# Kernel tuning notes

Measured on AMD Instinct MI355X. Metric: run time of the kernel, lower is better.

Reference implementation:

```python
import jax, jax.numpy as jnp
import numpy as np

N, DEG, FIN, FOUT, K = 50000, 16, 32, 64, 3
E = N * DEG


def setup_inputs() -> dict:
    key = jax.random.key(0)
    ks = jax.random.split(key, 10)
    rng = np.random.default_rng(0)
    # unique edges sorted row-major (src*N+dst), ring guarantees deg_in/out>0
    ring = np.arange(N, dtype=np.int64) * N + (np.arange(N, dtype=np.int64) + 1) % N
    cand = np.unique(rng.integers(0, N * N, size=3 * E, dtype=np.int64))
    cand = np.setdiff1d(cand, ring, assume_unique=True)[: E - N]
    codes = np.sort(np.concatenate([cand, ring]))
    assert codes.shape[0] == E
    edge_index = jnp.asarray(np.stack([codes // N, codes % N]).astype(np.int32))
    X = jax.random.normal(ks[0], (N, FIN), jnp.float32)
    edge_weight = jax.random.uniform(ks[1], (E,), jnp.float32, 0.5, 1.5)
    cin = FIN + FOUT
    xav = float(np.sqrt(6.0 / (cin + FOUT)))
    def w(k):
        return jax.random.uniform(k, (2, K, cin, FOUT), jnp.float32, -xav, xav)
    return {
        'X': X, 'edge_index': edge_index, 'edge_weight': edge_weight,
        'Wz': w(ks[2]), 'bz': jnp.zeros((FOUT,), jnp.float32),
        'Wr': w(ks[3]), 'br': jnp.zeros((FOUT,), jnp.float32),
        'Wh': w(ks[4]), 'bh': jnp.zeros((FOUT,), jnp.float32),
    }


def _dconv(X, src, dst, rev_src, rev_dst, norm_out, norm_in, W, b):
    n = X.shape[0]
    def prop(x, s, d, nrm):  # out[d] += nrm * x[s]
        return jax.ops.segment_sum(nrm[:, None] * x[s], d, num_segments=n)
    H = X @ W[0, 0] + X @ W[1, 0]
    if W.shape[1] > 1:
        Tx1o = prop(X, src, dst, norm_out)
        Tx1i = prop(X, rev_src, rev_dst, norm_in)
        H = H + Tx1o @ W[0, 1] + Tx1i @ W[1, 1]
        for k in range(2, W.shape[1]):
            Tx1o = 2.0 * prop(Tx1o, src, dst, norm_out) - X
            Tx1i = 2.0 * prop(Tx1i, rev_src, rev_dst, norm_in) - X
            H = H + Tx1o @ W[0, k] + Tx1i @ W[1, k]
    return H + b


def reference(X, edge_index, edge_weight, Wz, bz, Wr, br, Wh, bh):
    n = X.shape[0]
    src, dst = edge_index[0], edge_index[1]
    deg_out = jax.ops.segment_sum(edge_weight, src, num_segments=n)
    deg_in = jax.ops.segment_sum(edge_weight, dst, num_segments=n)
    # faithful to original: both norms indexed by row (source)
    norm_out = 1.0 / deg_out[src]
    norm_in = 1.0 / deg_in[src]
    # reverse edges in dense_to_sparse(adj.T) order: sorted by (dst, src)
    order = jnp.argsort(dst.astype(jnp.int64) * n + src.astype(jnp.int64))
    rev_src, rev_dst = dst[order], src[order]
    H = jnp.zeros((n, Wz.shape[-1]), X.dtype)
    dc = lambda inp, W, b: _dconv(inp, src, dst, rev_src, rev_dst, norm_out, norm_in, W, b)
    Z = jax.nn.sigmoid(dc(jnp.concatenate([X, H], axis=1), Wz, bz))
    R = jax.nn.sigmoid(dc(jnp.concatenate([X, H], axis=1), Wr, br))
    H_tilde = jnp.tanh(dc(jnp.concatenate([X, H * R], axis=1), Wh, bh))
    return Z * H + (1.0 - Z) * H_tilde
```

## Files before the change

### kernel.cpp

```cpp
#include <hip/hip_runtime.h>
#include <hip/hip_fp16.h>
#include <cmath>

#define NN 50000
#define NE 800000
#define PADF 96
#define NBIN 196
#define NBLK 391
#define FCAP 6144
#define DST_HI 42949
#define SRC_CUT 33648

__device__ __forceinline__ unsigned short f2h(float f) {
  __half h = __float2half_rn(f);
  return *reinterpret_cast<unsigned short*>(&h);
}

typedef _Float16 half4 __attribute__((ext_vector_type(4)));
typedef float f32x4 __attribute__((ext_vector_type(4)));

__global__ __launch_bounds__(256) void k_aux(const float* __restrict__ X, const int* __restrict__ src,
                                             const int* __restrict__ dst, const float* __restrict__ ew,
                                             int* __restrict__ H,
                                             int* __restrict__ rptr, float* __restrict__ dout,
                                             const float* __restrict__ Wz, const float* __restrict__ Wh,
                                             unsigned short* __restrict__ WT, unsigned short* __restrict__ Xh,
                                             int* __restrict__ s0g) {
  __shared__ int hh[256];
  __shared__ int s0l;
  int bid = blockIdx.x;
  int t = threadIdx.x;
  if (bid >= 667) {
    int h = bid - 667;
    hh[t] = 0;
    if (t == 0) s0l = 0;
    __syncthreads();
    int my = 0;
#pragma unroll
    for (int r = 0; r < 8; ++r) {
      int e = h * 2048 + r * 256 + t;
      if (e < NE) {
        int d = dst[e];
        atomicAdd(&hh[d >> 8], 1);
        my += (d < DST_HI) ? 1 : 0;
        my += (d == DST_HI && src[e] < SRC_CUT) ? 1 : 0;
      }
    }
    atomicAdd(&s0l, my);
    __syncthreads();
    if (t < NBIN) H[t * NBLK + h] = hh[t];
    if (t == 0) atomicAdd(s0g, s0l);
  } else if (bid < 196) {
    int i = bid * 256 + t;
    if (i >= NN) return;
    int lo = 0, hi = NE;
    while (lo < hi) { int m = (lo + hi) >> 1; if (src[m] < i) lo = m + 1; else hi = m; }
    int lo2 = lo, hi2 = NE;
    while (lo2 < hi2) { int m = (lo2 + hi2) >> 1; if (src[m] < i + 1) lo2 = m + 1; else hi2 = m; }
    rptr[i] = lo;
    if (i == NN - 1) rptr[NN] = lo2;
    float a = 0.f;
    for (int p = lo; p < lo2; ++p) a += ew[p];
    dout[i] = a;
  } else if (bid < 276) {
    int idx = (bid - 196) * 256 + t;
    int kk = idx >> 7, f = idx & 127;
    int blk = kk >> 5, c = kk & 31;
    const float* W = (f < 64) ? Wz : Wh;
    int fl = f & 63;
    float v;
    if (blk == 0)      v = W[c * 64 + fl] + W[18432 + c * 64 + fl];
    else if (blk == 1) v = W[6144 + c * 64 + fl];
    else if (blk == 2) v = W[18432 + 6144 + c * 64 + fl];
    else if (blk == 3) v = W[2 * 6144 + c * 64 + fl];
    else               v = W[18432 + 2 * 6144 + c * 64 + fl];
    WT[f * 160 + kk] = f2h(v);
  } else {
    int tt = (bid - 276) * 256 + t;
    int base = tt * 16;
    if (base >= NN * 32) return;
#pragma unroll
    for (int q = 0; q < 2; ++q) {
      const float4 a = *(const float4*)&X[base + q * 8];
      const float4 b = *(const float4*)&X[base + q * 8 + 4];
      ushort4 o1 = make_ushort4(f2h(a.x), f2h(a.y), f2h(a.z), f2h(a.w));
      ushort4 o2 = make_ushort4(f2h(b.x), f2h(b.y), f2h(b.z), f2h(b.w));
      *(ushort4*)&Xh[base + q * 8] = o1;
      *(ushort4*)&Xh[base + q * 8 + 4] = o2;
    }
  }
}

__global__ __launch_bounds__(512) void k_scanrow(int* __restrict__ H, int* __restrict__ rowtot) {
  __shared__ int tmp[512];
  int row = blockIdx.x;
  int t = threadIdx.x;
  int v = (t < NBLK) ? H[row * NBLK + t] : 0;
  tmp[t] = v;
  __syncthreads();
  for (int off = 1; off < 512; off <<= 1) {
    int u = (t >= (unsigned)off) ? tmp[t - off] : 0;
    __syncthreads();
    tmp[t] += u;
    __syncthreads();
  }
  if (t < NBLK) H[row * NBLK + t] = tmp[t] - v;
  if (t == 511) rowtot[row] = tmp[511];
}

__global__ __launch_bounds__(256) void k_part(const int* __restrict__ src, const int* __restrict__ dst,
                                              const int* __restrict__ P, const int* __restrict__ rowtot,
                                              unsigned long long* __restrict__ cmp64) {
  __shared__ int loc[NBIN];
  __shared__ int rs[256];
  __shared__ int rbase[NBIN];
  int h = blockIdx.x;
  int t = threadIdx.x;
  int v = (t < NBIN) ? rowtot[t] : 0;
  rs[t] = v;
  if (t < NBIN) loc[t] = 0;
  __syncthreads();
  for (int off = 1; off < 256; off <<= 1) {
    int u = (t >= (unsigned)off) ? rs[t - off] : 0;
    __syncthreads();
    rs[t] += u;
    __syncthreads();
  }
  if (t < NBIN) rbase[t] = rs[t] - v;
  __syncthreads();
#pragma unroll
  for (int r = 0; r < 8; ++r) {
    int e = h * 2048 + r * 256 + t;
    if (e < NE) {
      int d = dst[e];
      int bin = d >> 8;
      int rk = atomicAdd(&loc[bin], 1);
      int pos = rbase[bin] + P[bin * NBLK + h] + rk;
      cmp64[pos] = ((unsigned long long)(d & 255) << 48) |
                   ((unsigned long long)src[e] << 24) | (unsigned long long)e;
    }
  }
}

__global__ __launch_bounds__(1024) void k_fine(const int* __restrict__ rowtot, const float* __restrict__ ew,
                                               const unsigned long long* __restrict__ cmp64,
                                               const int* __restrict__ rawsrc, const float* __restrict__ dout,
                                               const int* __restrict__ s0g,
                                               int* __restrict__ sp, float* __restrict__ din,
                                               int2* __restrict__ cnf, int2* __restrict__ cnr) {
  __shared__ unsigned long long a1[FCAP], a2[FCAP];
  __shared__ int fh[256], fcnt[256], fo[257];
  __shared__ int bs[2];
  int cb = blockIdx.x;
  int t = threadIdx.x;
  if (t < 64) {
    int s = 0;
    for (int i = t; i < cb; i += 64) s += rowtot[i];
    s += __shfl_xor(s, 32, 64); s += __shfl_xor(s, 16, 64); s += __shfl_xor(s, 8, 64);
    s += __shfl_xor(s, 4, 64);  s += __shfl_xor(s, 2, 64);  s += __shfl_xor(s, 1, 64);
    if (t == 0) { bs[0] = s; bs[1] = s + rowtot[cb]; }
  }
  if (t < 256) { fh[t] = 0; fcnt[t] = 0; }
  __syncthreads();
  int base = bs[0];
  int m = bs[1] - base;
  if (m > FCAP) m = FCAP;
  for (int i = t; i < m; i += 1024) {
    unsigned long long it = cmp64[base + i];
    a1[i] = it;
    atomicAdd(&fh[(int)(it >> 48)], 1);
  }
  __syncthreads();
  if (t < 64) {
    int v0 = fh[t * 4], v1 = fh[t * 4 + 1], v2 = fh[t * 4 + 2], v3 = fh[t * 4 + 3];
    int s1 = v0 + v1, s2 = s1 + v2, tot = s2 + v3;
    int run = tot;
    for (int off = 1; off < 64; off <<= 1) {
      int v = __shfl_up(run, off, 64);
      if (t >= off) run += v;
    }
    int excl = run - tot;
    fo[t * 4] = excl; fo[t * 4 + 1] = excl + v0; fo[t * 4 + 2] = excl + s1; fo[t * 4 + 3] = excl + s2;
    if (t == 63) fo[256] = excl + tot;
  }
  __syncthreads();
  for (int i = t; i < m; i += 1024) {
    unsigned long long it = a1[i];
    int b = (int)(it >> 48);
    int p2 = fo[b] + atomicAdd(&fcnt[b], 1);
    a2[p2] = it;
  }
  if (t < 256) {
    int d = cb * 256 + t;
    if (d <= NN) sp[d] = base + fo[t];
  }
  {
    int d = cb * 256 + t;
    if (t < 257 && d == NN) sp[NN] = base + fo[t];
  }
  __syncthreads();
  const int s0 = s0g[0];
  const int wv0 = t >> 6, lane = t & 63;
  for (int seg = wv0; seg < 256; seg += 16) {
    int d = cb * 256 + seg;
    if (d >= NN) break;
    int f0 = fo[seg], f1 = fo[seg + 1];
    int n = f1 - f0;
    int b0g = base + f0;
    if (n > 64) {
      if (lane == 0) {
        unsigned long long arr[PADF];
        int nn = n > PADF ? PADF : n;
        for (int i = 0; i < nn; ++i) arr[i] = a2[f0 + i];
        for (int i = 1; i < nn; ++i) {
          unsigned long long v = arr[i]; int j = i - 1;
          while (j >= 0 && arr[j] > v) { arr[j + 1] = arr[j]; --j; }
          arr[j + 1] = v;
        }
        float s = 0.f;
        for (int i = 0; i < nn; ++i) {
          unsigned long long it = arr[i];
          int e = (int)(it & 0xFFFFFF);
          int sc = (int)((it >> 24) & 0xFFFF);
          s += ew[e];
          cnf[b0g + i] = make_int2(sc, __float_as_int(1.0f / dout[sc]));
          int j = b0g + i - s0; if (j < 0) j += NE;
          cnr[e] = make_int2(d, rawsrc[j]);
        }
        din[d] = s;
      }
      continue;
    }
    unsigned long long k = ~0ULL;
    if (lane < n) k = a2[f0 + lane];
    if (n > 1) {
#pragma unroll
      for (int kk = 2; kk <= 64; kk <<= 1) {
#pragma unroll
        for (int j = kk >> 1; j > 0; j >>= 1) {
          unsigned long long o = __shfl_xor(k, j, 64);
          bool lower = (lane & j) == 0;
          bool asc = (lane & kk) == 0;
          bool keepmin = (lower == asc);
          if (keepmin ? (o < k) : (o > k)) k = o;
        }
      }
    }
    float wsum = 0.f;
    if (lane < n) {
      int e = (int)(k & 0xFFFFFF);
      int sc = (int)((k >> 24) & 0xFFFF);
      wsum = ew[e];
      cnf[b0g + lane] = make_int2(sc, __float_as_int(1.0f / dout[sc]));
      int j = b0g + lane - s0; if (j < 0) j += NE;
      cnr[e] = make_int2(d, rawsrc[j]);
    }
    wsum += __shfl_xor(wsum, 32, 64); wsum += __shfl_xor(wsum, 16, 64);
    wsum += __shfl_xor(wsum, 8, 64);  wsum += __shfl_xor(wsum, 4, 64);
    wsum += __shfl_xor(wsum, 2, 64);  wsum += __shfl_xor(wsum, 1, 64);
    if (lane == 0) din[d] = wsum;
  }
}

__global__ __launch_bounds__(256) void k_prop2(const unsigned short* __restrict__ inA, const int* __restrict__ rpA,
                                               const int2* __restrict__ cnA, const float* __restrict__ wiA,
                                               unsigned short* __restrict__ outAh,
                                               const unsigned short* __restrict__ inB, const int* __restrict__ rpB,
                                               const int2* __restrict__ cnB, const float* __restrict__ wiB,
                                               unsigned short* __restrict__ outBh,
                                               const float* __restrict__ sub, float mul) {
  int t = blockIdx.x * 256 + threadIdx.x;
  const int half = NN * 8;
  const unsigned short* in; const int* rp; const int2* cn; const float* wi; unsigned short* outh;
  if (t < half) { in = inA; rp = rpA; cn = cnA; wi = wiA; outh = outAh; }
  else          { in = inB; rp = rpB; cn = cnB; wi = wiB; outh = outBh; t -= half; }
  int r = t >> 3;
  if (r >= NN) return;
  int lane8 = t & 7;
  int c4 = lane8 * 4;
  int b = rp[r], e2 = rp[r + 1];
  float a0[4] = {0.f, 0.f, 0.f, 0.f}, a1[4] = {0.f, 0.f, 0.f, 0.f};
  int p = b;
#define GATH(cc, ww) { \
    uint2 bv = *(const uint2*)&in[(cc) * 32 + c4]; \
    float2 f01 = __half22float2(*(const __half2*)&bv.x); \
    float2 f23 = __half22float2(*(const __half2*)&bv.y); \
    float* a = (jj & 1) ? a1 : a0; \
    a[0] += (ww) * f01.x; a[1] += (ww) * f01.y; \
    a[2] += (ww) * f23.x; a[3] += (ww) * f23.y; }
  for (; p + 16 <= e2; p += 16) {
    int2 u = cn[p + lane8];
    int2 v = cn[p + 8 + lane8];
    float uw = wi ? (1.0f / wi[u.y]) : __int_as_float(u.y);
    float vw = wi ? (1.0f / wi[v.y]) : __int_as_float(v.y);
#pragma unroll
    for (int jj = 0; jj < 8; ++jj) {
      int col = __shfl(u.x, jj, 8);
      float w = __shfl(uw, jj, 8);
      GATH(col, w)
    }
#pragma unroll
    for (int jj = 0; jj < 8; ++jj) {
      int col = __shfl(v.x, jj, 8);
      float w = __shfl(vw, jj, 8);
      GATH(col, w)
    }
  }
  for (; p + 8 <= e2; p += 8) {
    int2 u = cn[p + lane8];
    float uw = wi ? (1.0f / wi[u.y]) : __int_as_float(u.y);
#pragma unroll
    for (int jj = 0; jj < 8; ++jj) {
      int col = __shfl(u.x, jj, 8);
      float w = __shfl(uw, jj, 8);
      GATH(col, w)
    }
  }
  for (int jj = 0; p < e2; ++p) {
    int2 c1 = cn[p];
    float w = wi ? (1.0f / wi[c1.y]) : __int_as_float(c1.y);
    GATH(c1.x, w)
  }
#undef GATH
  float ax = a0[0] + a1[0], ay = a0[1] + a1[1], az = a0[2] + a1[2], aw = a0[3] + a1[3];
  float4 o;
  if (sub) {
    const float4 s = *(const float4*)&sub[r * 32 + c4];
    o.x = mul * ax - s.x; o.y = mul * ay - s.y; o.z = mul * az - s.z; o.w = mul * aw - s.w;
  } else {
    o.x = ax; o.y = ay; o.z = az; o.w = aw;
  }
  ushort4 oh = make_ushort4(f2h(o.x), f2h(o.y), f2h(o.z), f2h(o.w));
  *(ushort4*)&outh[r * 32 + c4] = oh;
}

__global__ __launch_bounds__(256) void k_gemm(const unsigned short* __restrict__ Xh,
                                              const unsigned short* __restrict__ T1oh,
                                              const unsigned short* __restrict__ T1ih,
                                              const unsigned short* __restrict__ T2oh,
                                              const unsigned short* __restrict__ T2ih,
                                              const unsigned short* __restrict__ WT,
                                              const float* __restrict__ bz, const float* __restrict__ bh,
                                              float* __restrict__ out) {
  __shared__ unsigned short wlds[128 * 168];
  const int tid = threadIdx.x;
  for (int i = tid; i < 128 * 20; i += 256) {
    int n = i / 20, o = i % 20;
    *(uint4*)&wlds[n * 168 + o * 8] = *(const uint4*)&WT[n * 160 + o * 8];
  }
  __syncthreads();
  const int l = tid & 63, wid = tid >> 6;
  const int m0 = wid * 16;
  const int rb = blockIdx.x * 64;
  int grow = rb + m0 + (l & 15); if (grow >= NN) grow = NN - 1;
  const int kg = (l >> 4) * 4;
  f32x4 acc[8];
#pragma unroll
  for (int t = 0; t < 8; ++t) acc[t] = (f32x4){0.f, 0.f, 0.f, 0.f};
  const unsigned short* srcs[5] = {Xh, T1oh, T1ih, T2oh, T2ih};
#pragma unroll
  for (int s = 0; s < 5; ++s) {
    const unsigned short* A = srcs[s];
#pragma unroll
    for (int h2 = 0; h2 < 2; ++h2) {
      const int kk = h2 * 16;
      half4 af = *(const half4*)&A[grow * 32 + kk + kg];
      const int kglob = s * 32 + kk + kg;
#pragma unroll
      for (int t = 0; t < 8; ++t) {
        half4 bf = *(const half4*)&wlds[(t * 16 + (l & 15)) * 168 + kglob];
        acc[t] = __builtin_amdgcn_mfma_f32_16x16x16f16(af, bf, acc[t], 0, 0, 0);
      }
    }
  }
  const int c = l & 15;
#pragma unroll
  for (int t = 0; t < 4; ++t) {
    int col = t * 16 + c;
    float bzv = bz[col], bhv = bh[col];
#pragma unroll
    for (int i = 0; i < 4; ++i) {
      int r = rb + m0 + (l >> 4) * 4 + i;
      if (r < NN) {
        float z = 1.f / (1.f + expf(-(acc[t][i] + bzv)));
        float hv = tanhf(acc[t + 4][i] + bhv);
        out[r * 64 + col] = (1.f - z) * hv;
      }
    }
  }
}

extern "C" void kernel_launch(void* const* d_in, const int* in_sizes, int n_in,
                              void* d_out, int out_size, void* d_ws, size_t ws_size,
                              hipStream_t stream) {
  const float* X  = (const float*)d_in[0];
  const int*   ei = (const int*)d_in[1];
  const float* ew = (const float*)d_in[2];
  const float* Wz = (const float*)d_in[3];
  const float* bz = (const float*)d_in[4];
  const float* Wh = (const float*)d_in[7];
  const float* bh = (const float*)d_in[8];
  float* out = (float*)d_out;
  const int* src = ei;
  const int* dst = ei + NE;

  char* p = (char*)d_ws;
  auto alloc = [&](size_t bytes) -> char* {
    char* r = p;
    p += (bytes + 255) & ~(size_t)255;
    return r;
  };
  unsigned short* Xh   = (unsigned short*)alloc((size_t)NN * 32 * 2);
  unsigned short* T1oh = (unsigned short*)alloc((size_t)NN * 32 * 2);
  unsigned short* T1ih = (unsigned short*)alloc((size_t)NN * 32 * 2);
  unsigned short* T2oh = (unsigned short*)alloc((size_t)NN * 32 * 2);
  unsigned short* T2ih = (unsigned short*)alloc((size_t)NN * 32 * 2);
  unsigned long long* cmp64 = (unsigned long long*)alloc((size_t)NE * 8);
  int2*  cnf     = (int2*)alloc((size_t)NE * 8);
  int2*  cnr     = (int2*)alloc((size_t)NE * 8);
  int*   H       = (int*)alloc((size_t)NBIN * NBLK * 4);
  int*   rowtot  = (int*)alloc(NBIN * 4);
  int*   sp      = (int*)alloc((NN + 1) * 4);
  int*   rptr    = (int*)alloc((NN + 1) * 4);
  float* dout    = (float*)alloc(NN * 4);
  float* din     = (float*)alloc(NN * 4);
  unsigned short* WT = (unsigned short*)alloc(128 * 160 * 2);
  int*   s0g     = (int*)alloc(256);

  hipMemsetAsync(s0g, 0, 4, stream);
  k_aux<<<1058, 256, 0, stream>>>(X, src, dst, ew, H, rptr, dout, Wz, Wh, WT, Xh, s0g);
  k_scanrow<<<NBIN, 512, 0, stream>>>(H, rowtot);
  k_part<<<NBLK, 256, 0, stream>>>(src, dst, H, rowtot, cmp64);
  k_fine<<<NBIN, 1024, 0, stream>>>(rowtot, ew, cmp64, src, dout, s0g, sp, din, cnf, cnr);

  k_prop2<<<3125, 256, 0, stream>>>(Xh, sp, cnf, nullptr, T1oh,
                                    Xh, rptr, cnr, din, T1ih, nullptr, 1.f);
  k_prop2<<<3125, 256, 0, stream>>>(T1oh, sp, cnf, nullptr, T2oh,
                                    T1ih, rptr, cnr, din, T2ih, X, 2.f);

  k_gemm<<<782, 256, 0, stream>>>(Xh, T1oh, T1ih, T2oh, T2ih, WT, bz, bh, out);
}
```

Before: 258.9 us.

## Split edge emission into separate kernel and precompute reverse-edge weights

k_fine now writes a compact (edge id, dst|src) record per sorted edge, and a new fully parallel k_emit kernel builds the forward and reverse CSR entries from it. Because din is complete by the time k_emit runs, it can store 1/din directly in the reverse entries. This removes the per-edge indirect load and reciprocal from both k_prop2 launches and takes the scattered writes out of the shared-memory-heavy k_fine. The cost is an extra launch and an extra 6.4MB intermediate buffer written and read back.

```diff
diff --git a/kernel.cpp b/kernel.cpp
--- a/kernel.cpp
+++ b/kernel.cpp
@@ -144,10 +144,8 @@
 
 __global__ __launch_bounds__(1024) void k_fine(const int* __restrict__ rowtot, const float* __restrict__ ew,
                                                const unsigned long long* __restrict__ cmp64,
-                                               const int* __restrict__ rawsrc, const float* __restrict__ dout,
-                                               const int* __restrict__ s0g,
-                                               int* __restrict__ sp, float* __restrict__ din,
-                                               int2* __restrict__ cnf, int2* __restrict__ cnr) {
+                                               int2* __restrict__ cmp, int* __restrict__ sp,
+                                               float* __restrict__ din) {
   __shared__ unsigned long long a1[FCAP], a2[FCAP];
   __shared__ int fh[256], fcnt[256], fo[257];
   __shared__ int bs[2];
@@ -199,7 +197,6 @@
     if (t < 257 && d == NN) sp[NN] = base + fo[t];
   }
   __syncthreads();
-  const int s0 = s0g[0];
   const int wv0 = t >> 6, lane = t & 63;
   for (int seg = wv0; seg < 256; seg += 16) {
     int d = cb * 256 + seg;
@@ -223,9 +220,7 @@
           int e = (int)(it & 0xFFFFFF);
           int sc = (int)((it >> 24) & 0xFFFF);
           s += ew[e];
-          cnf[b0g + i] = make_int2(sc, __float_as_int(1.0f / dout[sc]));
-          int j = b0g + i - s0; if (j < 0) j += NE;
-          cnr[e] = make_int2(d, rawsrc[j]);
+          cmp[b0g + i] = make_int2(e, (int)(((unsigned)d << 16) | (unsigned)sc));
         }
         din[d] = s;
       }
@@ -251,9 +246,7 @@
       int e = (int)(k & 0xFFFFFF);
       int sc = (int)((k >> 24) & 0xFFFF);
       wsum = ew[e];
-      cnf[b0g + lane] = make_int2(sc, __float_as_int(1.0f / dout[sc]));
-      int j = b0g + lane - s0; if (j < 0) j += NE;
-      cnr[e] = make_int2(d, rawsrc[j]);
+      cmp[b0g + lane] = make_int2(e, (int)(((unsigned)d << 16) | (unsigned)sc));
     }
     wsum += __shfl_xor(wsum, 32, 64); wsum += __shfl_xor(wsum, 16, 64);
     wsum += __shfl_xor(wsum, 8, 64);  wsum += __shfl_xor(wsum, 4, 64);
@@ -262,18 +255,31 @@
   }
 }
 
+__global__ __launch_bounds__(256) void k_emit(const int2* __restrict__ cmp, const int* __restrict__ rawsrc,
+                                              const float* __restrict__ dout, const float* __restrict__ din,
+                                              const int* __restrict__ s0g,
+                                              int2* __restrict__ cnf, int2* __restrict__ cnr) {
+  int i = blockIdx.x * 256 + threadIdx.x;
+  if (i >= NE) return;
+  int2 c = cmp[i];
+  int e = c.x;
+  unsigned y = (unsigned)c.y;
+  int d = (int)(y >> 16), sc = (int)(y & 0xFFFF);
+  cnf[i] = make_int2(sc, __float_as_int(1.0f / dout[sc]));
+  int j = i - s0g[0]; if (j < 0) j += NE;
+  cnr[e] = make_int2(d, __float_as_int(1.0f / din[rawsrc[j]]));
+}
+
 __global__ __launch_bounds__(256) void k_prop2(const unsigned short* __restrict__ inA, const int* __restrict__ rpA,
-                                               const int2* __restrict__ cnA, const float* __restrict__ wiA,
-                                               unsigned short* __restrict__ outAh,
+                                               const int2* __restrict__ cnA, unsigned short* __restrict__ outAh,
                                                const unsigned short* __restrict__ inB, const int* __restrict__ rpB,
-                                               const int2* __restrict__ cnB, const float* __restrict__ wiB,
-                                               unsigned short* __restrict__ outBh,
+                                               const int2* __restrict__ cnB, unsigned short* __restrict__ outBh,
                                                const float* __restrict__ sub, float mul) {
   int t = blockIdx.x * 256 + threadIdx.x;
   const int half = NN * 8;
-  const unsigned short* in; const int* rp; const int2* cn; const float* wi; unsigned short* outh;
-  if (t < half) { in = inA; rp = rpA; cn = cnA; wi = wiA; outh = outAh; }
-  else          { in = inB; rp = rpB; cn = cnB; wi = wiB; outh = outBh; t -= half; }
+  const unsigned short* in; const int* rp; const int2* cn; unsigned short* outh;
+  if (t < half) { in = inA; rp = rpA; cn = cnA; outh = outAh; }
+  else          { in = inB; rp = rpB; cn = cnB; outh = outBh; t -= half; }
   int r = t >> 3;
   if (r >= NN) return;
   int lane8 = t & 7;
@@ -291,34 +297,31 @@
   for (; p + 16 <= e2; p += 16) {
     int2 u = cn[p + lane8];
     int2 v = cn[p + 8 + lane8];
-    float uw = wi ? (1.0f / wi[u.y]) : __int_as_float(u.y);
-    float vw = wi ? (1.0f / wi[v.y]) : __int_as_float(v.y);
 #pragma unroll
     for (int jj = 0; jj < 8; ++jj) {
       int col = __shfl(u.x, jj, 8);
-      float w = __shfl(uw, jj, 8);
+      float w = __int_as_float(__shfl(u.y, jj, 8));
       GATH(col, w)
     }
 #pragma unroll
     for (int jj = 0; jj < 8; ++jj) {
       int col = __shfl(v.x, jj, 8);
-      float w = __shfl(vw, jj, 8);
+      float w = __int_as_float(__shfl(v.y, jj, 8));
       GATH(col, w)
     }
   }
   for (; p + 8 <= e2; p += 8) {
     int2 u = cn[p + lane8];
-    float uw = wi ? (1.0f / wi[u.y]) : __int_as_float(u.y);
 #pragma unroll
     for (int jj = 0; jj < 8; ++jj) {
       int col = __shfl(u.x, jj, 8);
-      float w = __shfl(uw, jj, 8);
+      float w = __int_as_float(__shfl(u.y, jj, 8));
       GATH(col, w)
     }
   }
   for (int jj = 0; p < e2; ++p) {
     int2 c1 = cn[p];
-    float w = wi ? (1.0f / wi[c1.y]) : __int_as_float(c1.y);
+    float w = __int_as_float(c1.y);
     GATH(c1.x, w)
   }
 #undef GATH
@@ -416,6 +419,7 @@
   unsigned short* T2oh = (unsigned short*)alloc((size_t)NN * 32 * 2);
   unsigned short* T2ih = (unsigned short*)alloc((size_t)NN * 32 * 2);
   unsigned long long* cmp64 = (unsigned long long*)alloc((size_t)NE * 8);
+  int2*  cmp     = (int2*)alloc((size_t)NE * 8);
   int2*  cnf     = (int2*)alloc((size_t)NE * 8);
   int2*  cnr     = (int2*)alloc((size_t)NE * 8);
   int*   H       = (int*)alloc((size_t)NBIN * NBLK * 4);
@@ -431,12 +435,13 @@
   k_aux<<<1058, 256, 0, stream>>>(X, src, dst, ew, H, rptr, dout, Wz, Wh, WT, Xh, s0g);
   k_scanrow<<<NBIN, 512, 0, stream>>>(H, rowtot);
   k_part<<<NBLK, 256, 0, stream>>>(src, dst, H, rowtot, cmp64);
-  k_fine<<<NBIN, 1024, 0, stream>>>(rowtot, ew, cmp64, src, dout, s0g, sp, din, cnf, cnr);
-
-  k_prop2<<<3125, 256, 0, stream>>>(Xh, sp, cnf, nullptr, T1oh,
-                                    Xh, rptr, cnr, din, T1ih, nullptr, 1.f);
-  k_prop2<<<3125, 256, 0, stream>>>(T1oh, sp, cnf, nullptr, T2oh,
-                                    T1ih, rptr, cnr, din, T2ih, X, 2.f);
+  k_fine<<<NBIN, 1024, 0, stream>>>(rowtot, ew, cmp64, cmp, sp, din);
+  k_emit<<<3125, 256, 0, stream>>>(cmp, src, dout, din, s0g, cnf, cnr);
+
+  k_prop2<<<3125, 256, 0, stream>>>(Xh, sp, cnf, T1oh,
+                                    Xh, rptr, cnr, T1ih, nullptr, 1.f);
+  k_prop2<<<3125, 256, 0, stream>>>(T1oh, sp, cnf, T2oh,
+                                    T1ih, rptr, cnr, T2ih, X, 2.f);
 
   k_gemm<<<782, 256, 0, stream>>>(Xh, T1oh, T1ih, T2oh, T2ih, WT, bz, bh, out);
 }
```

Result: no change. 258.2 us (-0.3%).
